# Optimization experiments

Hardware: AMD Instinct MI355X
Metric: run time of the kernel (lower is better)

The kernel has to match this reference:

```python
import jax, jax.numpy as jnp
import numpy as np

N_NODES = 20000
IN_CH = 7
HID = 256
HEADS = 8
NEG_SLOPE = 0.2


def glorot(key, shape):
    fan = shape[0] + shape[-1] if len(shape) == 2 else int(np.prod(shape))
    lim = jnp.sqrt(6.0 / fan)
    return jax.random.uniform(key, shape, jnp.float32, -lim, lim)


def setup_inputs() -> dict:
    key = jax.random.key(0)
    ks = jax.random.split(key, 12)
    x = jax.random.normal(ks[0], (N_NODES, IN_CH), jnp.float32)
    edge_index = jax.random.randint(ks[1], (2, 160000), 0, N_NODES, jnp.int64)
    # conv1: in=7 -> heads=8, out=256, concat
    W1 = glorot(ks[2], (IN_CH, HEADS * HID))
    att_src1 = glorot(ks[3], (HEADS, HID))
    att_dst1 = glorot(ks[4], (HEADS, HID))
    b1 = jnp.zeros((HEADS * HID,), jnp.float32)
    # conv2: in=2048 -> heads=1, out=256, mean (concat=False)
    W2 = glorot(ks[5], (HEADS * HID, 1 * HID))
    att_src2 = glorot(ks[6], (1, HID))
    att_dst2 = glorot(ks[7], (1, HID))
    b2 = jnp.zeros((HID,), jnp.float32)
    return {"x": x, "edge_index": edge_index, "W1": W1, "att_src1": att_src1,
            "att_dst1": att_dst1, "b1": b1, "W2": W2, "att_src2": att_src2,
            "att_dst2": att_dst2, "b2": b2}


def gat_conv(x, src, dst, W, att_src, att_dst, bias, concat):
    # PyG GATConv (eval mode, dropout disabled)
    H, C = att_src.shape
    n = x.shape[0]
    h = (x @ W).reshape(n, H, C)                      # [N,H,C]
    a_src = jnp.sum(h * att_src[None], axis=-1)       # [N,H]
    a_dst = jnp.sum(h * att_dst[None], axis=-1)       # [N,H]
    alpha = a_src[src] + a_dst[dst]                   # [E,H]
    alpha = jax.nn.leaky_relu(alpha, NEG_SLOPE)
    # segment softmax over incoming edges of each destination node
    amax = jax.ops.segment_max(alpha, dst, num_segments=n)
    alpha = jnp.exp(alpha - amax[dst])
    denom = jax.ops.segment_sum(alpha, dst, num_segments=n)
    alpha = alpha / (denom[dst] + 1e-16)
    msg = h[src] * alpha[:, :, None]                  # [E,H,C] gather + weight
    out = jax.ops.segment_sum(msg, dst, num_segments=n)  # scatter-add aggregate
    out = out.reshape(n, H * C) if concat else out.mean(axis=1)
    return out + bias


def reference(x, edge_index, W1, att_src1, att_dst1, b1, W2, att_src2, att_dst2, b2):
    n = x.shape[0]
    # PyG GATConv default: add self-loops
    loops = jnp.arange(n, dtype=edge_index.dtype)
    src = jnp.concatenate([edge_index[0], loops])
    dst = jnp.concatenate([edge_index[1], loops])
    h = gat_conv(x, src, dst, W1, att_src1, att_dst1, b1, concat=True)
    h = jax.nn.elu(h)
    out = gat_conv(h, src, dst, W2, att_src2, att_dst2, b2, concat=False)
    return out
```

## Files before the change

### kernel.cpp

```cpp
#include <hip/hip_runtime.h>
#include <hip/hip_bf16.h>

#define N_NODES 20000
#define E_ORIG  160000
#define E_TOT   180000
#define HEADS   8
#define HID     256
#define F1      2048
#define NEG     0.2f
#define MAXDEG  96
#define GBKS    32
#define BMG     80

typedef __attribute__((ext_vector_type(8))) short  short8;
typedef __attribute__((ext_vector_type(4))) short  short4_;
typedef __attribute__((ext_vector_type(4))) float  f32x4;

__device__ inline float bf2f(ushort u){ union{unsigned u32; float f;} v; v.u32=((unsigned)u)<<16; return v.f; }
__device__ inline ushort f2bf(float f){
  union{float f; unsigned u;} v; v.f=f;
  unsigned lsb=(v.u>>16)&1u; v.u += 0x7fffu + lsb; return (ushort)(v.u>>16);
}

__device__ inline void gload16(const ushort* g, ushort* s){
  __builtin_amdgcn_global_load_lds((const __attribute__((address_space(1))) unsigned int*)g,
                                   (__attribute__((address_space(3))) unsigned int*)s, 16, 0, 0);
}

__global__ __launch_bounds__(256) void k_pre(const float* __restrict__ x, const float* __restrict__ W1,
    const float* __restrict__ as1, const float* __restrict__ ad1, const float* __restrict__ W2,
    float* __restrict__ a_src1, float* __restrict__ a_dst1, ushort* __restrict__ W2bT,
    int* __restrict__ cnt){
  __shared__ float s_w[128];
  __shared__ ushort sh[256][65];
  int tid = threadIdx.x, bid = blockIdx.x;
  if (tid < 128){
    int t = tid & 63;
    int k = t>>3, i = t&7;
    float v = 0.f;
    if (i < 7){
      const float* wp = W1 + i*F1 + (k<<8);
      const float* ap = ((tid<64) ? as1 : ad1) + (k<<8);
      f32x4 a4 = {0,0,0,0};
      for (int c=0;c<256;c+=4)
        a4 += (*(const f32x4*)&wp[c]) * (*(const f32x4*)&ap[c]);
      v = a4[0]+a4[1]+a4[2]+a4[3];
    }
    s_w[tid] = v;
  }
  __syncthreads();
  {
    int nl = tid>>3, k = tid&7;
    int n = bid*32 + nl;
    if (n < N_NODES){
      float s=0.f, d=0.f;
      const float* ws = &s_w[k*8];
      const float* wd = &s_w[64+k*8];
#pragma unroll
      for (int i=0;i<7;i++){
        float xv = x[n*7+i];
        s += xv*ws[i]; d += xv*wd[i];
      }
      a_src1[n*8+k]=s; a_dst1[n*8+k]=d;
    }
  }
  if (bid >= 32 && bid < 111){
    int i = (bid-32)*256 + tid;
    if (i < N_NODES) cnt[i] = 0;
  }
  if (bid < 32){
    int k0 = bid*64;
    for (int kk=0; kk<64; kk++) sh[tid][kk] = f2bf(W2[(size_t)(k0+kk)*256 + tid]);
    __syncthreads();
#pragma unroll
    for (int c8=0; c8<8; c8++){
      short8 v;
#pragma unroll
      for (int j=0;j<8;j++) v[j] = (short)sh[tid][c8*8+j];
      *(short8*)&W2bT[(size_t)tid*F1 + k0 + c8*8] = v;
    }
  }
}

__global__ void k_scat(const int* __restrict__ ei, int* __restrict__ cnt, int* __restrict__ bucket){
  int e = blockIdx.x*256 + threadIdx.x;
  if (e >= E_TOT) return;
  int s, d;
  if (e < E_ORIG){ s = ei[e]; d = ei[E_ORIG + e]; }
  else           { s = d = e - E_ORIG; }
  int pos = atomicAdd(&cnt[d], 1);
  if (pos < MAXDEG) bucket[d*MAXDEG + pos] = s;
}

__global__ __launch_bounds__(512) void k_sa1(const int* __restrict__ cnt, const int* __restrict__ bucket,
    const float* __restrict__ a_src1, const float* __restrict__ a_dst1,
    const float* __restrict__ x, const float* __restrict__ W1, const float* __restrict__ b1,
    ushort* __restrict__ x2){
  __shared__ float sxa[8][64];
  int tid = threadIdx.x, wv = tid>>6, lane = tid&63;
  int n = blockIdx.x*8 + wv;
  {
    int k = lane>>3, i = lane&7;
    int ie = (i==7)?0:i;
    int base = n*MAXDEG;
    int deg  = cnt[n]; if (deg>MAXDEG) deg=MAXDEG;
    float ad = a_dst1[n*8+k];
    int src0 = (lane<deg)    ? bucket[base+lane]    : 0;
    int src1 = (lane+64<deg) ? bucket[base+lane+64] : 0;
    float denom = 0.f, acc = 0.f;
    int j = 0;
    for (; j+4<=deg; j+=4){
      int s0 = (j<64)   ? __shfl(src0,j)   : __shfl(src1,j-64);
      int s1 = (j+1<64) ? __shfl(src0,j+1) : __shfl(src1,j-63);
      int s2 = (j+2<64) ? __shfl(src0,j+2) : __shfl(src1,j-62);
      int s3 = (j+3<64) ? __shfl(src0,j+3) : __shfl(src1,j-61);
      float A0 = a_src1[(size_t)s0*8+k];
      float A1 = a_src1[(size_t)s1*8+k];
      float A2 = a_src1[(size_t)s2*8+k];
      float A3 = a_src1[(size_t)s3*8+k];
      float X0 = x[(size_t)s0*7+ie];
      float X1 = x[(size_t)s1*7+ie];
      float X2 = x[(size_t)s2*7+ie];
      float X3 = x[(size_t)s3*7+ie];
      A0 += ad; A1 += ad; A2 += ad; A3 += ad;
      A0 = (A0>0.f)?A0:NEG*A0;  A1 = (A1>0.f)?A1:NEG*A1;
      A2 = (A2>0.f)?A2:NEG*A2;  A3 = (A3>0.f)?A3:NEG*A3;
      float w0 = __expf(A0), w1 = __expf(A1), w2 = __expf(A2), w3 = __expf(A3);
      denom += w0; acc += w0*X0;
      denom += w1; acc += w1*X1;
      denom += w2; acc += w2*X2;
      denom += w3; acc += w3*X3;
    }
    for (; j<deg; j++){
      int s0 = (j<64) ? __shfl(src0,j) : __shfl(src1,j-64);
      float A0 = a_src1[(size_t)s0*8+k] + ad;
      A0 = (A0>0.f)?A0:NEG*A0;
      float w0 = __expf(A0);
      denom += w0; acc += w0*x[(size_t)s0*7+ie];
    }
    sxa[wv][lane] = acc/denom;
  }
  __syncthreads();
  int kh = tid>>6, c4 = (tid&63)<<2;
  f32x4 w1r[7];
#pragma unroll
  for (int i=0;i<7;i++) w1r[i] = *(const f32x4*)(W1 + i*F1 + (kh<<8) + c4);
  f32x4 bb = *(const f32x4*)(b1 + (kh<<8) + c4);
#pragma unroll
  for (int g=0; g<8; g++){
    int nn = blockIdx.x*8 + g;
    const float* xa = &sxa[g][kh<<3];
    f32x4 h = bb;
#pragma unroll
    for (int i=0;i<7;i++) h += xa[i]*w1r[i];
    short4_ o;
#pragma unroll
    for (int j=0;j<4;j++){ float v=h[j]; v=(v>0.f)?v:(__expf(v)-1.f); o[j]=(short)f2bf(v); }
    *(short4_*)(x2 + (size_t)nn*F1 + (kh<<8) + c4) = o;
  }
}

__global__ __launch_bounds__(256) void k_gemm2m(const ushort* __restrict__ A,
    const ushort* __restrict__ BT, ushort* __restrict__ h2b,
    const float* __restrict__ as2, const float* __restrict__ ad2,
    float* __restrict__ a_src2, float* __restrict__ a_dst2){
  __shared__ __align__(16) ushort S[2][(BMG+256)*64];
  int tid = threadIdx.x;
  int m0 = blockIdx.x*BMG;
  int w = tid>>6, l = tid&63;
  int lrow = l&15, lk = l>>4;
  int nc = w<<6;

  const ushort* gp[11];
#pragma unroll
  for (int rep=0;rep<11;rep++){
    int lin = rep*256 + tid;
    if (lin < BMG*8){
      int r = lin>>3, s = lin&7;
      gp[rep] = A + (size_t)(m0+r)*F1 + ((s ^ (r&7))<<3);
    } else if (lin < (BMG+256)*8){
      int j = lin - BMG*8;
      int c = j>>3, s = j&7;
      gp[rep] = BT + (size_t)c*F1 + ((s ^ (c&7))<<3);
    } else gp[rep] = BT;
  }

  f32x4 acc[5][4] = {};

#pragma unroll
  for (int rep=0;rep<10;rep++) gload16(gp[rep], &S[0][(rep*256+tid)<<3]);
  if (tid < 128) gload16(gp[10], &S[0][(10*256+tid)<<3]);
  __syncthreads();

  int cur = 0;
  for (int t=0; t<GBKS; t++){
    if (t+1 < GBKS){
      int k0 = (t+1)<<6;
#pragma unroll
      for (int rep=0;rep<10;rep++) gload16(gp[rep]+k0, &S[cur^1][(rep*256+tid)<<3]);
      if (tid < 128) gload16(gp[10]+k0, &S[cur^1][(10*256+tid)<<3]);
    }
    const ushort* as_ = &S[cur][0];
    const ushort* bs_ = &S[cur][BMG*64];
#pragma unroll
    for (int kk=0;kk<2;kk++){
      short8 af[5], bfr[4];
#pragma unroll
      for (int m=0;m<5;m++){
        int r = (m<<4) + lrow;
        af[m] = *(const short8*)&as_[(r<<6) + ((((kk<<2)|lk) ^ (r&7))<<3)];
      }
#pragma unroll
      for (int n=0;n<4;n++){
        int c = nc + (n<<4) + lrow;
        bfr[n] = *(const short8*)&bs_[(c<<6) + ((((kk<<2)|lk) ^ (c&7))<<3)];
      }
#pragma unroll
      for (int m=0;m<5;m++)
#pragma unroll
        for (int n=0;n<4;n++)
          acc[m][n] = __builtin_amdgcn_mfma_f32_16x16x32_bf16(af[m], bfr[n], acc[m][n], 0,0,0);
    }
    __syncthreads();
    cur ^= 1;
  }

  float* sps = (float*)&S[0][0];
  float* spd = sps + BMG*4;
  float s2v[4], d2v[4];
#pragma unroll
  for (int n=0;n<4;n++){
    int col = nc + (n<<4) + lrow;
    s2v[n]=as2[col]; d2v[n]=ad2[col];
  }
#pragma unroll
  for (int m=0;m<5;m++){
#pragma unroll
    for (int j=0;j<4;j++){
      int lr = (m<<4) + (lk<<2) + j;
      int grow = m0 + lr;
      float ps=0.f, pd=0.f;
#pragma unroll
      for (int n=0;n<4;n++){
        float v = acc[m][n][j];
        ps += v*s2v[n]; pd += v*d2v[n];
        h2b[(size_t)grow*256 + nc+(n<<4)+lrow] = f2bf(v);
      }
      ps += __shfl_xor(ps,8); ps += __shfl_xor(ps,4); ps += __shfl_xor(ps,2); ps += __shfl_xor(ps,1);
      pd += __shfl_xor(pd,8); pd += __shfl_xor(pd,4); pd += __shfl_xor(pd,2); pd += __shfl_xor(pd,1);
      if (lrow==0){
        sps[(lr<<2) | w] = ps;
        spd[(lr<<2) | w] = pd;
      }
    }
  }
  __syncthreads();
  if (tid < BMG){
    int grow = m0 + tid;
    f32x4 a = *(const f32x4*)&sps[tid<<2];
    f32x4 b = *(const f32x4*)&spd[tid<<2];
    a_src2[grow] = a[0]+a[1]+a[2]+a[3];
    a_dst2[grow] = b[0]+b[1]+b[2]+b[3];
  }
}

__global__ __launch_bounds__(512) void k_agg2(const int* __restrict__ cnt, const int* __restrict__ bucket,
    const float* __restrict__ a_src2, const float* __restrict__ a_dst2, const ushort* __restrict__ h2b,
    const float* __restrict__ b2, float* __restrict__ out){
  int tid = threadIdx.x, wv = tid>>6, lane = tid&63;
  int n = blockIdx.x*8 + wv;
  int base = n*MAXDEG;
  int deg  = cnt[n]; if (deg > MAXDEG) deg = MAXDEG;
  float ad = a_dst2[n];

  int src0 = (lane<deg)     ? bucket[base+lane]    : 0;
  int src1 = (lane+64<deg)  ? bucket[base+lane+64] : 0;
  float e0 = 0.f, e1 = 0.f;
  if (lane<deg)   { float a = a_src2[src0]+ad; a = (a>0.f)?a:NEG*a; e0 = __expf(a); }
  if (lane+64<deg){ float a = a_src2[src1]+ad; a = (a>0.f)?a:NEG*a; e1 = __expf(a); }
  float s = e0+e1;
  for (int off=32; off; off>>=1) s += __shfl_xor(s,off);
  float inv = 1.f/(s+1e-16f);
  e0 *= inv; e1 *= inv;

  int c0 = lane<<2;
  float acc0=0.f, acc1=0.f, acc2=0.f, acc3=0.f;
  int d1 = (deg<64)?deg:64;
  for (int j=0;j<d1;j++){
    float w = __shfl(e0, j);
    int  sj = __shfl(src0, j);
    short4_ hv = *(const short4_*)(h2b + (size_t)sj*256 + c0);
    acc0 += w*bf2f((ushort)hv[0]); acc1 += w*bf2f((ushort)hv[1]);
    acc2 += w*bf2f((ushort)hv[2]); acc3 += w*bf2f((ushort)hv[3]);
  }
  for (int j=64;j<deg;j++){
    float w = __shfl(e1, j-64);
    int  sj = __shfl(src1, j-64);
    short4_ hv = *(const short4_*)(h2b + (size_t)sj*256 + c0);
    acc0 += w*bf2f((ushort)hv[0]); acc1 += w*bf2f((ushort)hv[1]);
    acc2 += w*bf2f((ushort)hv[2]); acc3 += w*bf2f((ushort)hv[3]);
  }
  f32x4 bb = *(const f32x4*)(b2 + c0);
  f32x4 o; o[0]=acc0+bb[0]; o[1]=acc1+bb[1]; o[2]=acc2+bb[2]; o[3]=acc3+bb[3];
  *(f32x4*)(out + (size_t)n*256 + c0) = o;
}

extern "C" void kernel_launch(void* const* d_in, const int* in_sizes, int n_in,
                              void* d_out, int out_size, void* d_ws, size_t ws_size,
                              hipStream_t stream){
  const float* x      = (const float*)d_in[0];
  const int*   ei     = (const int*)  d_in[1];
  const float* W1     = (const float*)d_in[2];
  const float* att_s1 = (const float*)d_in[3];
  const float* att_d1 = (const float*)d_in[4];
  const float* b1     = (const float*)d_in[5];
  const float* W2     = (const float*)d_in[6];
  const float* att_s2 = (const float*)d_in[7];
  const float* att_d2 = (const float*)d_in[8];
  const float* b2     = (const float*)d_in[9];
  float* out = (float*)d_out;

  char* p = (char*)d_ws;
  auto alloc = [&](size_t bytes)->char*{ char* r = p; p += (bytes + 255) & ~(size_t)255; return r; };
  ushort* x2    = (ushort*)alloc((size_t)N_NODES*F1*2);
  ushort* W2bT  = (ushort*)alloc((size_t)F1*256*2);
  ushort* h2b   = (ushort*)alloc((size_t)N_NODES*256*2);
  float*  a_src1= (float*) alloc((size_t)N_NODES*8*4);
  float*  a_dst1= (float*) alloc((size_t)N_NODES*8*4);
  float*  a_src2= (float*) alloc((size_t)N_NODES*4);
  float*  a_dst2= (float*) alloc((size_t)N_NODES*4);
  int*    cnt   = (int*)   alloc((size_t)N_NODES*4);
  int*    bucket= (int*)   alloc((size_t)N_NODES*MAXDEG*4);

  k_pre    <<<(N_NODES+31)/32, 256, 0, stream>>>(x, W1, att_s1, att_d1, W2,
                                                 a_src1, a_dst1, W2bT, cnt);
  k_scat   <<<(E_TOT+255)/256, 256, 0, stream>>>(ei, cnt, bucket);
  k_sa1    <<<N_NODES/8, 512, 0, stream>>>(cnt, bucket, a_src1, a_dst1, x, W1, b1, x2);
  k_gemm2m <<<N_NODES/BMG, 256, 0, stream>>>(x2, W2bT, h2b, att_s2, att_d2, a_src2, a_dst2);
  k_agg2   <<<N_NODES/8, 512, 0, stream>>>(cnt, bucket, a_src2, a_dst2, h2b, b2, out);
}
```

Before: 118.5 us.

## Warp-specialize GEMM2 into producer loader waves and consumer MFMA waves

The second-layer GEMM kernel goes from 256 to 512 threads. Four extra waves act as producers that issue the global-to-LDS loads for the next K tile and wait on them, while the original four waves only run MFMAs out of the current LDS buffer. The two groups hand off through raw s_barrier calls each iteration. This aims to take load issue and vmcnt waits off the compute waves' critical path. In exchange it doubles block size, which may lower occupancy, and it relies on careful barrier matching between the two groups.

New measurement: 117.2 us. About the same (-1.1%).

```diff
diff --git a/kernel.cpp b/kernel.cpp
--- a/kernel.cpp
+++ b/kernel.cpp
@@ -160,7 +160,7 @@
   }
 }
 
-__global__ __launch_bounds__(256) void k_gemm2m(const ushort* __restrict__ A,
+__global__ __launch_bounds__(512) void k_gemm2m(const ushort* __restrict__ A,
     const ushort* __restrict__ BT, ushort* __restrict__ h2b,
     const float* __restrict__ as2, const float* __restrict__ ad2,
     float* __restrict__ a_src2, float* __restrict__ a_dst2){
@@ -169,88 +169,104 @@
   int m0 = blockIdx.x*BMG;
   int w = tid>>6, l = tid&63;
   int lrow = l&15, lk = l>>4;
-  int nc = w<<6;
-
-  const ushort* gp[11];
-#pragma unroll
-  for (int rep=0;rep<11;rep++){
-    int lin = rep*256 + tid;
-    if (lin < BMG*8){
-      int r = lin>>3, s = lin&7;
-      gp[rep] = A + (size_t)(m0+r)*F1 + ((s ^ (r&7))<<3);
-    } else if (lin < (BMG+256)*8){
-      int j = lin - BMG*8;
-      int c = j>>3, s = j&7;
-      gp[rep] = BT + (size_t)c*F1 + ((s ^ (c&7))<<3);
-    } else gp[rep] = BT;
-  }
+  int nc = (w&3)<<6;
 
   f32x4 acc[5][4] = {};
 
-#pragma unroll
-  for (int rep=0;rep<10;rep++) gload16(gp[rep], &S[0][(rep*256+tid)<<3]);
-  if (tid < 128) gload16(gp[10], &S[0][(10*256+tid)<<3]);
-  __syncthreads();
-
-  int cur = 0;
-  for (int t=0; t<GBKS; t++){
-    if (t+1 < GBKS){
-      int k0 = (t+1)<<6;
-#pragma unroll
-      for (int rep=0;rep<10;rep++) gload16(gp[rep]+k0, &S[cur^1][(rep*256+tid)<<3]);
-      if (tid < 128) gload16(gp[10]+k0, &S[cur^1][(10*256+tid)<<3]);
-    }
-    const ushort* as_ = &S[cur][0];
-    const ushort* bs_ = &S[cur][BMG*64];
-#pragma unroll
-    for (int kk=0;kk<2;kk++){
-      short8 af[5], bfr[4];
-#pragma unroll
-      for (int m=0;m<5;m++){
-        int r = (m<<4) + lrow;
-        af[m] = *(const short8*)&as_[(r<<6) + ((((kk<<2)|lk) ^ (r&7))<<3)];
-      }
-#pragma unroll
-      for (int n=0;n<4;n++){
-        int c = nc + (n<<4) + lrow;
-        bfr[n] = *(const short8*)&bs_[(c<<6) + ((((kk<<2)|lk) ^ (c&7))<<3)];
-      }
-#pragma unroll
-      for (int m=0;m<5;m++)
-#pragma unroll
-        for (int n=0;n<4;n++)
-          acc[m][n] = __builtin_amdgcn_mfma_f32_16x16x32_bf16(af[m], bfr[n], acc[m][n], 0,0,0);
-    }
-    __syncthreads();
-    cur ^= 1;
+  if (w >= 4){
+    int pt = tid - 256;
+    const ushort* gp[11];
+    bool act[11];
+#pragma unroll
+    for (int rep=0;rep<11;rep++){
+      int lin = rep*256 + pt;
+      act[rep] = lin < (BMG+256)*8;
+      int linc = act[rep] ? lin : 0;
+      if (linc < BMG*8){
+        int r = linc>>3, s = linc&7;
+        gp[rep] = A + (size_t)(m0+r)*F1 + ((s ^ (r&7))<<3);
+      } else {
+        int j = linc - BMG*8;
+        int c = j>>3, s = j&7;
+        gp[rep] = BT + (size_t)c*F1 + ((s ^ (c&7))<<3);
+      }
+    }
+#pragma unroll
+    for (int rep=0;rep<11;rep++)
+      if (act[rep]) gload16(gp[rep], &S[0][(rep*256+pt)<<3]);
+    asm volatile("s_waitcnt vmcnt(0)" ::: "memory");
+    __builtin_amdgcn_s_barrier();
+    __builtin_amdgcn_sched_barrier(0);
+    for (int t=0; t<GBKS; t++){
+      if (t+1 < GBKS){
+        int k0 = (t+1)<<6;
+        ushort* dst = &S[(t+1)&1][0];
+#pragma unroll
+        for (int rep=0;rep<11;rep++)
+          if (act[rep]) gload16(gp[rep]+k0, &dst[(rep*256+pt)<<3]);
+        asm volatile("s_waitcnt vmcnt(0)" ::: "memory");
+      }
+      __builtin_amdgcn_s_barrier();
+      __builtin_amdgcn_sched_barrier(0);
+    }
+  } else {
+    __builtin_amdgcn_s_barrier();
+    __builtin_amdgcn_sched_barrier(0);
+    for (int t=0; t<GBKS; t++){
+      const ushort* as_ = &S[t&1][0];
+      const ushort* bs_ = &S[t&1][BMG*64];
+#pragma unroll
+      for (int kk=0;kk<2;kk++){
+        short8 af[5], bfr[4];
+#pragma unroll
+        for (int m=0;m<5;m++){
+          int r = (m<<4) + lrow;
+          af[m] = *(const short8*)&as_[(r<<6) + ((((kk<<2)|lk) ^ (r&7))<<3)];
+        }
+#pragma unroll
+        for (int n=0;n<4;n++){
+          int c = nc + (n<<4) + lrow;
+          bfr[n] = *(const short8*)&bs_[(c<<6) + ((((kk<<2)|lk) ^ (c&7))<<3)];
+        }
+#pragma unroll
+        for (int m=0;m<5;m++)
+#pragma unroll
+          for (int n=0;n<4;n++)
+            acc[m][n] = __builtin_amdgcn_mfma_f32_16x16x32_bf16(af[m], bfr[n], acc[m][n], 0,0,0);
+      }
+      __builtin_amdgcn_s_barrier();
+      __builtin_amdgcn_sched_barrier(0);
+    }
   }
 
   float* sps = (float*)&S[0][0];
   float* spd = sps + BMG*4;
-  float s2v[4], d2v[4];
-#pragma unroll
-  for (int n=0;n<4;n++){
-    int col = nc + (n<<4) + lrow;
-    s2v[n]=as2[col]; d2v[n]=ad2[col];
-  }
-#pragma unroll
-  for (int m=0;m<5;m++){
-#pragma unroll
-    for (int j=0;j<4;j++){
-      int lr = (m<<4) + (lk<<2) + j;
-      int grow = m0 + lr;
-      float ps=0.f, pd=0.f;
-#pragma unroll
-      for (int n=0;n<4;n++){
-        float v = acc[m][n][j];
-        ps += v*s2v[n]; pd += v*d2v[n];
-        h2b[(size_t)grow*256 + nc+(n<<4)+lrow] = f2bf(v);
-      }
-      ps += __shfl_xor(ps,8); ps += __shfl_xor(ps,4); ps += __shfl_xor(ps,2); ps += __shfl_xor(ps,1);
-      pd += __shfl_xor(pd,8); pd += __shfl_xor(pd,4); pd += __shfl_xor(pd,2); pd += __shfl_xor(pd,1);
-      if (lrow==0){
-        sps[(lr<<2) | w] = ps;
-        spd[(lr<<2) | w] = pd;
+  if (w < 4){
+    float s2v[4], d2v[4];
+#pragma unroll
+    for (int n=0;n<4;n++){
+      int col = nc + (n<<4) + lrow;
+      s2v[n]=as2[col]; d2v[n]=ad2[col];
+    }
+#pragma unroll
+    for (int m=0;m<5;m++){
+#pragma unroll
+      for (int j=0;j<4;j++){
+        int lr = (m<<4) + (lk<<2) + j;
+        int grow = m0 + lr;
+        float ps=0.f, pd=0.f;
+#pragma unroll
+        for (int n=0;n<4;n++){
+          float v = acc[m][n][j];
+          ps += v*s2v[n]; pd += v*d2v[n];
+          h2b[(size_t)grow*256 + nc+(n<<4)+lrow] = f2bf(v);
+        }
+        ps += __shfl_xor(ps,8); ps += __shfl_xor(ps,4); ps += __shfl_xor(ps,2); ps += __shfl_xor(ps,1);
+        pd += __shfl_xor(pd,8); pd += __shfl_xor(pd,4); pd += __shfl_xor(pd,2); pd += __shfl_xor(pd,1);
+        if (lrow==0){
+          sps[(lr<<2) | w] = ps;
+          spd[(lr<<2) | w] = pd;
+        }
       }
     }
   }
@@ -336,6 +352,6 @@
                                                  a_src1, a_dst1, W2bT, cnt);
   k_scat   <<<(E_TOT+255)/256, 256, 0, stream>>>(ei, cnt, bucket);
   k_sa1    <<<N_NODES/8, 512, 0, stream>>>(cnt, bucket, a_src1, a_dst1, x, W1, b1, x2);
-  k_gemm2m <<<N_NODES/BMG, 256, 0, stream>>>(x2, W2bT, h2b, att_s2, att_d2, a_src2, a_dst2);
+  k_gemm2m <<<N_NODES/BMG, 512, 0, stream>>>(x2, W2bT, h2b, att_s2, att_d2, a_src2, a_dst2);
   k_agg2   <<<N_NODES/8, 512, 0, stream>>>(cnt, bucket, a_src2, a_dst2, h2b, b2, out);
 }
```
